# Performance work log

Hardware: AMD Instinct MI355X
Metric: run time of the kernel (lower is better)

The kernel has to match this reference:

```python
import jax, jax.numpy as jnp
import numpy as np

B, S, HID = 2, 2048, 2048
H, KV, D = 16, 4, 128          # query heads, kv heads, head_dim
G = H // KV                     # q heads per kv head
RD = 32                         # rotary_dim = int(0.25 * 128), even
THETA = 5000000.0
EPS = 1e-6


def _rms_norm(x, w):
    # out = x * rsqrt(mean(x^2)) * (1 + w)   (weight is zero-init)
    out = x * jax.lax.rsqrt(jnp.mean(x * x, axis=-1, keepdims=True) + EPS)
    return out * (1.0 + w.astype(x.dtype))


def _apply_rope(x, positions):
    # x: [B,S,h,RD]; standard HF rope with rotate_half on the rotary slice
    half = RD // 2
    inv_freq = 1.0 / (THETA ** (jnp.arange(0, half, dtype=jnp.float32) * 2.0 / RD))
    freqs = positions.astype(jnp.float32)[..., None] * inv_freq  # [B,S,half]
    emb = jnp.concatenate([freqs, freqs], axis=-1)               # [B,S,RD]
    cos = jnp.cos(emb)[:, :, None, :].astype(x.dtype)
    sin = jnp.sin(emb)[:, :, None, :].astype(x.dtype)
    x1, x2 = x[..., :half], x[..., half:]
    rot = jnp.concatenate([-x2, x1], axis=-1)
    return x * cos + rot * sin


def _partial_rope(q, k, positions):
    q_rot, q_pass = q[..., :RD], q[..., RD:]
    k_rot, k_pass = k[..., :RD], k[..., RD:]
    q_rot = _apply_rope(q_rot, positions)
    k_rot = _apply_rope(k_rot, positions)
    return (jnp.concatenate([q_rot, q_pass], axis=-1),
            jnp.concatenate([k_rot, k_pass], axis=-1))


def setup_inputs() -> dict:
    k0, k1, k2 = jax.random.split(jax.random.key(0), 3)
    x = jax.random.normal(k0, (B, S, HID), dtype=jnp.float32)
    positions = jnp.broadcast_to(jnp.arange(S, dtype=jnp.int32), (B, S))
    attention_mask = jnp.ones((B, S), dtype=bool)
    wqkv = jax.random.normal(k1, (HID, (H * 2 + 2 * KV) * D), dtype=jnp.float32) * 0.02
    wo = jax.random.normal(k2, (H * D, HID), dtype=jnp.float32) * 0.02
    q_norm_w = jnp.zeros((D,), dtype=jnp.float32)
    k_norm_w = jnp.zeros((D,), dtype=jnp.float32)
    return {"x": x, "positions": positions, "attention_mask": attention_mask,
            "wqkv": wqkv, "wo": wo, "q_norm_w": q_norm_w, "k_norm_w": k_norm_w}


def reference(x, positions, attention_mask, wqkv, wo, q_norm_w, k_norm_w):
    bsz, seq, _ = x.shape
    qkv = jnp.einsum('bsh,hf->bsf', x, wqkv)  # [B,S,5120]
    q_sz, kv_sz = H * 2 * D, KV * D
    q_raw = qkv[..., :q_sz]
    k_raw = qkv[..., q_sz:q_sz + kv_sz]
    v_raw = qkv[..., q_sz + kv_sz:]

    q_all = q_raw.reshape(bsz, seq, H, 2 * D)
    q, gate = jnp.split(q_all, 2, axis=-1)          # each [B,S,H,D]
    gate = gate.reshape(bsz, seq, H * D)

    q = _rms_norm(q, q_norm_w)
    k = _rms_norm(k_raw.reshape(bsz, seq, KV, D), k_norm_w)
    v = v_raw.reshape(bsz, seq, KV, D)
    q, k = _partial_rope(q, k, positions)

    # GQA causal attention, scale = 1/sqrt(head_dim)
    qg = q.reshape(bsz, seq, KV, G, D)
    scores = jnp.einsum('bqkgd,bskd->bkgqs', qg, k) * (1.0 / np.sqrt(D))
    causal = jnp.tril(jnp.ones((seq, seq), dtype=bool))
    mask = causal[None, None, None] & attention_mask[:, None, None, None, :]
    scores = jnp.where(mask, scores, jnp.finfo(scores.dtype).min)
    probs = jax.nn.softmax(scores, axis=-1)
    attn = jnp.einsum('bkgqs,bskd->bqkgd', probs, v)
    attn = attn.reshape(bsz, seq, H * D)

    attn = attn * jax.nn.sigmoid(gate)
    return jnp.einsum('bsf,fh->bsh', attn, wo)
```

## Files before the change

### kernel.cpp

```cpp
#include <hip/hip_runtime.h>

typedef unsigned short u16;
typedef unsigned int u32;
typedef __attribute__((ext_vector_type(8))) short short8;
typedef __attribute__((ext_vector_type(4))) float floatx4;

#define SEQ   2048
#define HIDD  2048
#define NQH   16
#define NKV   4
#define HDIM  128
#define QKV_N 5120
#define K_OFF 4096
#define V_OFF 4608
#define NTOK  4096
#define PSTR  40

__device__ __forceinline__ float b2f(u16 u) {
  u32 x = ((u32)u) << 16;
  return __builtin_bit_cast(float, x);
}
__device__ __forceinline__ u16 f2b(float f) {
  u32 x = __builtin_bit_cast(u32, f);
  u32 r = x + 0x7fffu + ((x >> 16) & 1u);
  return (u16)(r >> 16);
}
__device__ __forceinline__ short8 pack8(floatx4 a, floatx4 b) {
  short8 s;
#pragma unroll
  for (int j = 0; j < 4; j++) { s[j] = (short)f2b(a[j]); s[4 + j] = (short)f2b(b[j]); }
  return s;
}
__device__ __forceinline__ void async_copy16(const u16* g, u16* lds) {
  __builtin_amdgcn_global_load_lds((const __attribute__((address_space(1))) u32*)g,
                                   (__attribute__((address_space(3))) u32*)lds, 16, 0, 0);
}

__global__ __launch_bounds__(256) void cast_bf16(const float* __restrict__ in,
                                                 u16* __restrict__ out, int n8) {
  const int i = blockIdx.x * 256 + threadIdx.x;
  if (i < n8) {
    const floatx4 f0 = *(const floatx4*)(in + (size_t)i * 8);
    const floatx4 f1 = *(const floatx4*)(in + (size_t)i * 8 + 4);
    *(short8*)(out + (size_t)i * 8) = pack8(f0, f1);
  }
}

__global__ __launch_bounds__(256) void transpose_f32_bf16(const float* __restrict__ in,
                                                          u16* __restrict__ out,
                                                          int R, int C) {
  __shared__ float tile[32][33];
  const int bx = blockIdx.x * 32;
  const int by = blockIdx.y * 32;
  const int tx = threadIdx.x & 31;
  const int ty = threadIdx.x >> 5;
#pragma unroll
  for (int i = ty; i < 32; i += 8)
    tile[i][tx] = in[(size_t)(by + i) * C + bx + tx];
  __syncthreads();
#pragma unroll
  for (int i = ty; i < 32; i += 8)
    out[(size_t)(bx + i) * R + by + tx] = f2b(tile[tx][i]);
}

__global__ __launch_bounds__(256) void pack_kv(const u16* __restrict__ qkv,
                                               u16* __restrict__ Kc,
                                               u16* __restrict__ Vp) {
  __shared__ u16 tile[32][136];
  const int t0 = blockIdx.x * 32;
  const int kv = blockIdx.y;
  const int tid = threadIdx.x;
  const int b  = t0 / SEQ;
  const int tl = t0 - b * SEQ;
  const int jt = tl >> 5;
  const size_t kvbase = (size_t)(b * NKV + kv) * SEQ * HDIM;

  const int row  = tid >> 3;
  const int part = tid & 7;
  const size_t qbase = (size_t)(t0 + row) * QKV_N;
  const short8 kv0 = *(const short8*)(qkv + qbase + K_OFF + kv * HDIM + part * 16);
  const short8 kv1 = *(const short8*)(qkv + qbase + K_OFF + kv * HDIM + part * 16 + 8);
  *(short8*)(Kc + kvbase + (size_t)(tl + row) * HDIM + part * 16)     = kv0;
  *(short8*)(Kc + kvbase + (size_t)(tl + row) * HDIM + part * 16 + 8) = kv1;
  const short8 vv0 = *(const short8*)(qkv + qbase + V_OFF + kv * HDIM + part * 16);
  const short8 vv1 = *(const short8*)(qkv + qbase + V_OFF + kv * HDIM + part * 16 + 8);
  *(short8*)&tile[row][part * 16]     = vv0;
  *(short8*)&tile[row][part * 16 + 8] = vv1;
  __syncthreads();
  const int d = tid >> 1;
  const int half = tid & 1;
  u16* vout = Vp + kvbase + (size_t)jt * HDIM * 32 + d * 32 + half * 16;
  short8 o0;
#pragma unroll
  for (int i = 0; i < 8; i++) o0[i] = (short)tile[half * 16 + i][d];
  short8 o1;
#pragma unroll
  for (int i = 0; i < 8; i++) o1[i] = (short)tile[half * 16 + 8 + i][d];
  *(short8*)(vout) = o0;
  *(short8*)(vout + 8) = o1;
}

template <bool C32>
__global__ __launch_bounds__(512, 2) void gemm_bt8(const u16* __restrict__ A,
                                                   const u16* __restrict__ Bt,
                                                   void* __restrict__ Cp,
                                                   int M, int N, int K) {
  __shared__ __align__(16) u16 As[2][256 * 64];
  __shared__ __align__(16) u16 Bs[2][256 * 64];
  const int tid  = threadIdx.x;
  const int wave = tid >> 6;
  const int lane = tid & 63;
  const int lm   = lane & 15;
  const int lq   = lane >> 4;
  const int nwg = gridDim.x * gridDim.y;
  const int bid = blockIdx.y * gridDim.x + blockIdx.x;
  const int sbid = (bid & 7) * (nwg >> 3) + (bid >> 3);
  const int m0   = (sbid / gridDim.x) * 256;
  const int n0   = (sbid % gridDim.x) * 256;
  const int wr   = wave >> 2;
  const int wc   = wave & 3;
  const int NK   = K >> 6;

  const int r0 = wave * 16 + (lane >> 3);
  const int c0 = (((lane & 7) ^ (r0 & 7)) << 3);
  const int dls = wave * 1024;

  auto stageA = [&](int buf, int kt, int h) {
    const u16* g = A + (size_t)(m0 + h * 128 + r0) * K + kt * 64 + c0;
    async_copy16(g,                &As[buf][h * 8192 + dls]);
    async_copy16(g + (size_t)8 * K, &As[buf][h * 8192 + dls + 512]);
  };
  auto stageB = [&](int buf, int kt, int h) {
    const u16* g = Bt + (size_t)(n0 + h * 128 + r0) * K + kt * 64 + c0;
    async_copy16(g,                &Bs[buf][h * 8192 + dls]);
    async_copy16(g + (size_t)8 * K, &Bs[buf][h * 8192 + dls + 512]);
  };
  auto rdA = [&](int buf, int row, int ch) {
    return *(const short8*)&As[buf][row * 64 + ((ch ^ (row & 7)) << 3)];
  };
  auto rdB = [&](int buf, int row, int ch) {
    return *(const short8*)&Bs[buf][row * 64 + ((ch ^ (row & 7)) << 3)];
  };

  floatx4 acc[8][4] = {};
  short8 aF[4][2], bF[4][2];

  stageA(0, 0, 0); stageA(0, 0, 1);
  stageB(0, 0, 0); stageB(0, 0, 1);
  stageB(1, 1, 0); stageB(1, 1, 1);
  asm volatile("s_waitcnt vmcnt(4)" ::: "memory");
  __builtin_amdgcn_sched_barrier(0);
  __builtin_amdgcn_s_barrier();

  for (int j = 0; j < NK; ++j) {
    const int cur = j & 1;
#pragma unroll
    for (int m = 0; m < 4; ++m)
#pragma unroll
      for (int kk = 0; kk < 2; ++kk)
        aF[m][kk] = rdA(cur, wr * 128 + m * 16 + lm, kk * 4 + lq);
#pragma unroll
    for (int n = 0; n < 2; ++n)
#pragma unroll
      for (int kk = 0; kk < 2; ++kk)
        bF[n][kk] = rdB(cur, wc * 64 + n * 16 + lm, kk * 4 + lq);
    if (j + 1 < NK) stageA(cur ^ 1, j + 1, 0);
    __builtin_amdgcn_s_barrier();
    asm volatile("s_waitcnt lgkmcnt(0)" ::: "memory");
    __builtin_amdgcn_sched_barrier(0);
    __builtin_amdgcn_s_setprio(1);
#pragma unroll
    for (int m = 0; m < 4; ++m)
#pragma unroll
      for (int n = 0; n < 2; ++n)
#pragma unroll
        for (int kk = 0; kk < 2; ++kk)
          acc[m][n] = __builtin_amdgcn_mfma_f32_16x16x32_bf16(aF[m][kk], bF[n][kk], acc[m][n], 0, 0, 0);
    __builtin_amdgcn_s_setprio(0);
    __builtin_amdgcn_s_barrier();
#pragma unroll
    for (int n = 0; n < 2; ++n)
#pragma unroll
      for (int kk = 0; kk < 2; ++kk)
        bF[2 + n][kk] = rdB(cur, wc * 64 + (2 + n) * 16 + lm, kk * 4 + lq);
    if (j + 1 < NK) stageA(cur ^ 1, j + 1, 1);
    __builtin_amdgcn_s_barrier();
    asm volatile("s_waitcnt lgkmcnt(0)" ::: "memory");
    __builtin_amdgcn_sched_barrier(0);
    __builtin_amdgcn_s_setprio(1);
#pragma unroll
    for (int m = 0; m < 4; ++m)
#pragma unroll
      for (int n = 0; n < 2; ++n)
#pragma unroll
        for (int kk = 0; kk < 2; ++kk)
          acc[m][2 + n] = __builtin_amdgcn_mfma_f32_16x16x32_bf16(aF[m][kk], bF[2 + n][kk], acc[m][2 + n], 0, 0, 0);
    __builtin_amdgcn_s_setprio(0);
    __builtin_amdgcn_s_barrier();
#pragma unroll
    for (int m = 0; m < 4; ++m)
#pragma unroll
      for (int kk = 0; kk < 2; ++kk)
        aF[m][kk] = rdA(cur, wr * 128 + 64 + m * 16 + lm, kk * 4 + lq);
    if (j + 2 < NK) stageB(cur, j + 2, 0);
    __builtin_amdgcn_s_barrier();
    asm volatile("s_waitcnt lgkmcnt(0)" ::: "memory");
    __builtin_amdgcn_sched_barrier(0);
    __builtin_amdgcn_s_setprio(1);
#pragma unroll
    for (int m = 0; m < 4; ++m)
#pragma unroll
      for (int n = 0; n < 2; ++n)
#pragma unroll
        for (int kk = 0; kk < 2; ++kk)
          acc[4 + m][n] = __builtin_amdgcn_mfma_f32_16x16x32_bf16(aF[m][kk], bF[n][kk], acc[4 + m][n], 0, 0, 0);
    __builtin_amdgcn_s_setprio(0);
    __builtin_amdgcn_s_barrier();
    if (j + 2 < NK) stageB(cur, j + 2, 1);
    __builtin_amdgcn_s_barrier();
    __builtin_amdgcn_s_setprio(1);
#pragma unroll
    for (int m = 0; m < 4; ++m)
#pragma unroll
      for (int n = 0; n < 2; ++n)
#pragma unroll
        for (int kk = 0; kk < 2; ++kk)
          acc[4 + m][2 + n] = __builtin_amdgcn_mfma_f32_16x16x32_bf16(aF[m][kk], bF[2 + n][kk], acc[4 + m][2 + n], 0, 0, 0);
    __builtin_amdgcn_s_setprio(0);
    if (j + 2 < NK) asm volatile("s_waitcnt vmcnt(4)" ::: "memory");
    else            asm volatile("s_waitcnt vmcnt(0)" ::: "memory");
    __builtin_amdgcn_sched_barrier(0);
    __builtin_amdgcn_s_barrier();
  }

#pragma unroll
  for (int mi = 0; mi < 8; ++mi)
#pragma unroll
    for (int ni = 0; ni < 4; ++ni)
#pragma unroll
      for (int r = 0; r < 4; ++r) {
        const int row = m0 + wr * 128 + mi * 16 + lq * 4 + r;
        const int col = n0 + wc * 64 + ni * 16 + lm;
        if (C32) ((float*)Cp)[(size_t)row * N + col] = acc[mi][ni][r];
        else     ((u16*)Cp)[(size_t)row * N + col] = f2b(acc[mi][ni][r]);
      }
}

template <bool C32>
__global__ __launch_bounds__(512, 2) void gemm_n128(const u16* __restrict__ A,
                                                    const u16* __restrict__ Bt,
                                                    void* __restrict__ Cp,
                                                    int M, int N, int K) {
  __shared__ __align__(16) u16 As[2][256 * 64];
  __shared__ __align__(16) u16 Bs[2][128 * 64];
  const int tid  = threadIdx.x;
  const int wave = tid >> 6;
  const int lane = tid & 63;
  const int lm   = lane & 15;
  const int lq   = lane >> 4;
  const int nwg = gridDim.x * gridDim.y;
  const int bid = blockIdx.y * gridDim.x + blockIdx.x;
  const int sbid = (bid & 7) * (nwg >> 3) + (bid >> 3);
  const int m0   = (sbid / gridDim.x) * 256;
  const int n0   = (sbid % gridDim.x) * 128;
  const int wr   = wave >> 1;
  const int wc   = wave & 1;
  const int NK   = K >> 6;

  auto stA = [&](int buf, int kt, int L) {
    const int cd  = L * 512 + wave * 64 + lane;
    const int row = cd >> 3;
    const int ch  = cd & 7;
    async_copy16(A + (size_t)(m0 + row) * K + kt * 64 + ((ch ^ (row & 7)) << 3),
                 &As[buf][(L * 512 + wave * 64) * 8]);
  };
  auto stB = [&](int buf, int kt, int L) {
    const int cd  = L * 512 + wave * 64 + lane;
    const int row = cd >> 3;
    const int ch  = cd & 7;
    async_copy16(Bt + (size_t)(n0 + row) * K + kt * 64 + ((ch ^ (row & 7)) << 3),
                 &Bs[buf][(L * 512 + wave * 64) * 8]);
  };
  auto rdA = [&](int buf, int row, int ch) {
    return *(const short8*)&As[buf][row * 64 + ((ch ^ (row & 7)) << 3)];
  };
  auto rdB = [&](int buf, int row, int ch) {
    return *(const short8*)&Bs[buf][row * 64 + ((ch ^ (row & 7)) << 3)];
  };

  floatx4 acc[4][4] = {};
  short8 aF[4][2], bF[4][2];

  stA(0, 0, 0); stA(0, 0, 1); stA(0, 0, 2); stA(0, 0, 3);
  stB(0, 0, 0); stB(0, 0, 1);
  stB(1, 1, 0); stB(1, 1, 1);
  asm volatile("s_waitcnt vmcnt(2)" ::: "memory");
  __builtin_amdgcn_sched_barrier(0);
  __builtin_amdgcn_s_barrier();

  for (int j = 0; j < NK; ++j) {
    const int cur = j & 1;
#pragma unroll
    for (int m = 0; m < 4; ++m)
#pragma unroll
      for (int kk = 0; kk < 2; ++kk)
        aF[m][kk] = rdA(cur, wr * 64 + m * 16 + lm, kk * 4 + lq);
#pragma unroll
    for (int n = 0; n < 4; ++n)
#pragma unroll
      for (int kk = 0; kk < 2; ++kk)
        bF[n][kk] = rdB(cur, wc * 64 + n * 16 + lm, kk * 4 + lq);
    if (j + 1 < NK) { stA(cur ^ 1, j + 1, 0); stA(cur ^ 1, j + 1, 1); }
    asm volatile("s_waitcnt lgkmcnt(8)" ::: "memory");
    __builtin_amdgcn_s_barrier();
    asm volatile("s_waitcnt lgkmcnt(0)" ::: "memory");
    __builtin_amdgcn_sched_barrier(0);
    __builtin_amdgcn_s_setprio(1);
#pragma unroll
    for (int m = 0; m < 4; ++m)
#pragma unroll
      for (int n = 0; n < 2; ++n)
#pragma unroll
        for (int kk = 0; kk < 2; ++kk)
          acc[m][n] = __builtin_amdgcn_mfma_f32_16x16x32_bf16(aF[m][kk], bF[n][kk], acc[m][n], 0, 0, 0);
    __builtin_amdgcn_s_setprio(0);
    __builtin_amdgcn_s_barrier();
    if (j + 1 < NK) { stA(cur ^ 1, j + 1, 2); stA(cur ^ 1, j + 1, 3); }
    if (j + 2 < NK) { stB(cur, j + 2, 0); stB(cur, j + 2, 1); }
    __builtin_amdgcn_s_barrier();
    __builtin_amdgcn_sched_barrier(0);
    __builtin_amdgcn_s_setprio(1);
#pragma unroll
    for (int m = 0; m < 4; ++m)
#pragma unroll
      for (int n = 0; n < 2; ++n)
#pragma unroll
        for (int kk = 0; kk < 2; ++kk)
          acc[m][2 + n] = __builtin_amdgcn_mfma_f32_16x16x32_bf16(aF[m][kk], bF[2 + n][kk], acc[m][2 + n], 0, 0, 0);
    __builtin_amdgcn_s_setprio(0);
    if (j + 2 < NK) asm volatile("s_waitcnt vmcnt(2)" ::: "memory");
    else            asm volatile("s_waitcnt vmcnt(0)" ::: "memory");
    __builtin_amdgcn_sched_barrier(0);
    __builtin_amdgcn_s_barrier();
  }

#pragma unroll
  for (int mi = 0; mi < 4; ++mi)
#pragma unroll
    for (int ni = 0; ni < 4; ++ni)
#pragma unroll
      for (int r = 0; r < 4; ++r) {
        const int row = m0 + wr * 64 + mi * 16 + lq * 4 + r;
        const int col = n0 + wc * 64 + ni * 16 + lm;
        if (C32) ((float*)Cp)[(size_t)row * N + col] = acc[mi][ni][r];
        else     ((u16*)Cp)[(size_t)row * N + col] = f2b(acc[mi][ni][r]);
      }
}

__global__ __launch_bounds__(64) void postproc(u16* __restrict__ qkv,
                                               const int* __restrict__ positions,
                                               const float* __restrict__ qw,
                                               const float* __restrict__ kw) {
  const int tok  = blockIdx.x;
  const int u    = blockIdx.y;
  const int lane = threadIdx.x;
  const float* w;
  int base;
  if (u < NQH) { base = u * 256; w = qw; }
  else         { base = K_OFF + (u - NQH) * HDIM; w = kw; }
  u16* p = qkv + (size_t)tok * QKV_N + base;
  const int d0 = lane * 2;
  float v0 = b2f(p[d0]);
  float v1 = b2f(p[d0 + 1]);
  float ss = v0 * v0 + v1 * v1;
#pragma unroll
  for (int off = 32; off >= 1; off >>= 1) ss += __shfl_xor(ss, off, 64);
  const float rs = rsqrtf(ss * (1.0f / 128.0f) + 1e-6f);
  v0 = v0 * rs * (1.0f + w[d0]);
  v1 = v1 * rs * (1.0f + w[d0 + 1]);
  const float pv0 = __shfl_xor(v0, 8, 64);
  const float pv1 = __shfl_xor(v1, 8, 64);
  if (d0 < 32) {
    const float fpos = (float)positions[tok];
    const int i = d0 & 15;
    const float inv0 = __powf(5.0e6f, -((float)i) / 16.0f);
    const float inv1 = __powf(5.0e6f, -((float)(i + 1)) / 16.0f);
    float s0, c0, s1, c1;
    sincosf(fpos * inv0, &s0, &c0);
    sincosf(fpos * inv1, &s1, &c1);
    if (d0 < 16) { v0 = v0 * c0 - pv0 * s0; v1 = v1 * c1 - pv1 * s1; }
    else         { v0 = v0 * c0 + pv0 * s0; v1 = v1 * c1 + pv1 * s1; }
  }
  if (u < NQH) {
    v0 *= 0.08838834764831845f;
    v1 *= 0.08838834764831845f;
  }
  p[d0]     = f2b(v0);
  p[d0 + 1] = f2b(v1);
}

__global__ __launch_bounds__(256) void attn_kernel(const u16* __restrict__ qkv,
                                                   const u16* __restrict__ Kc,
                                                   const u16* __restrict__ Vp,
                                                   u16* __restrict__ attn_g) {
  __shared__ __align__(16) u16 Ks[2][4][32][32];
  __shared__ __align__(16) u16 Vs[2][128][32];
  __shared__ __align__(16) u16 P_lds[4][16 * PSTR];
  const int tid  = threadIdx.x;
  const int wave = tid >> 6;
  const int lane = tid & 63;
  const int lm = lane & 15;
  const int lq = lane >> 4;
  const int kvi = blockIdx.y;
  const int b   = blockIdx.z;
  const int h   = kvi * 4 + wave;
  const size_t tokbase = (size_t)b * SEQ;
  const size_t kvbase  = (size_t)(b * NKV + kvi) * SEQ * HDIM;
  const int klocal = lane >> 2;
  const int ssw = ((lane & 3) ^ ((lane >> 3) & 3)) * 8;
  const int rsw = (lq ^ ((lm >> 1) & 3)) * 8;

  short8 onesF;
#pragma unroll
  for (int j = 0; j < 8; j++) onesF[j] = (short)0x3F80;

  auto stage = [&](int buf, int j) {
    const u16* ksrc = Kc + kvbase + (size_t)j * 32 * HDIM;
#pragma unroll
    for (int half = 0; half < 2; half++)
      async_copy16(ksrc + (size_t)(half * 16 + klocal) * HDIM + wave * 32 + ssw,
                   &Ks[buf][wave][half * 16][0]);
    const u16* vsrc = Vp + kvbase + (size_t)j * (HDIM * 32);
#pragma unroll
    for (int i = 0; i < 2; i++)
      async_copy16(vsrc + wave * 1024 + i * 512 + (lane >> 2) * 32 + ssw,
                   &Vs[buf][wave * 32 + i * 16][0]);
  };

  auto run_tile = [&](int t) {
    short8 qF[4];
    const u16* qp = qkv + (tokbase + 16 * t + lm) * QKV_N + h * 256;
#pragma unroll
    for (int kc = 0; kc < 4; kc++)
      qF[kc] = *(const short8*)(qp + kc * 32 + lq * 8);

    floatx4 O[8] = {};
    floatx4 lacc = {};
    const int jmax = t >> 1;
    const int moff = (t & 1) * 16;

    __syncthreads();
    stage(0, 0);
    for (int j = 0; j <= jmax; j++) {
      const int cur = j & 1;
      __syncthreads();
      if (j < jmax) stage(cur ^ 1, j + 1);
      short8 kF[2][4], vF[8];
#pragma unroll
      for (int n0 = 0; n0 < 2; n0++)
#pragma unroll
        for (int kc = 0; kc < 4; kc++)
          kF[n0][kc] = *(const short8*)&Ks[cur][kc][n0 * 16 + lm][rsw];
#pragma unroll
      for (int dc = 0; dc < 8; dc++)
        vF[dc] = *(const short8*)&Vs[cur][dc * 16 + lm][rsw];

      floatx4 Sc[2] = {};
#pragma unroll
      for (int n0 = 0; n0 < 2; n0++)
#pragma unroll
        for (int kc = 0; kc < 4; kc++)
          Sc[n0] = __builtin_amdgcn_mfma_f32_16x16x32_bf16(qF[kc], kF[n0][kc], Sc[n0], 0, 0, 0);

      const bool masked = (j == jmax);
#pragma unroll
      for (int n0 = 0; n0 < 2; n0++)
#pragma unroll
        for (int r = 0; r < 4; r++) {
          float pe = __expf(Sc[n0][r]);
          if (masked) {
            const int rowloc = lq * 4 + r;
            const int keyloc = n0 * 16 + lm;
            pe = (keyloc <= rowloc + moff) ? pe : 0.0f;
          }
          P_lds[wave][(lq * 4 + r) * PSTR + n0 * 16 + lm] = f2b(pe);
        }
      const short8 pF = *(const short8*)&P_lds[wave][lm * PSTR + lq * 8];
      lacc = __builtin_amdgcn_mfma_f32_16x16x32_bf16(pF, onesF, lacc, 0, 0, 0);
#pragma unroll
      for (int dc = 0; dc < 8; dc++)
        O[dc] = __builtin_amdgcn_mfma_f32_16x16x32_bf16(pF, vF[dc], O[dc], 0, 0, 0);
    }

#pragma unroll
    for (int r = 0; r < 4; r++) {
      const int row = 16 * t + lq * 4 + r;
      const size_t tok = tokbase + row;
      const float inv_l = 1.0f / lacc[r];
#pragma unroll
      for (int dc = 0; dc < 8; dc++) {
        const int d = dc * 16 + lm;
        const float g = b2f(qkv[tok * QKV_N + h * 256 + 128 + d]);
        const float sg = 1.0f / (1.0f + __expf(-g));
        attn_g[tok * HIDD + h * HDIM + d] = f2b(O[dc][r] * inv_l * sg);
      }
    }
  };

  const int p = blockIdx.x;
  run_tile(p);
  run_tile(127 - p);
}

extern "C" void kernel_launch(void* const* d_in, const int* in_sizes, int n_in,
                              void* d_out, int out_size, void* d_ws, size_t ws_size,
                              hipStream_t stream) {
  const float* x        = (const float*)d_in[0];
  const int* positions  = (const int*)d_in[1];
  const float* wqkv     = (const float*)d_in[3];
  const float* wo       = (const float*)d_in[4];
  const float* qnw      = (const float*)d_in[5];
  const float* knw      = (const float*)d_in[6];
  float* out = (float*)d_out;

  char* ws = (char*)d_ws;
  u16* qkv    = (u16*)(ws);
  u16* wqkv_t = (u16*)(ws + 41943040);
  u16* attn_g = (u16*)(ws + 41943040);
  u16* Kc     = (u16*)(ws + 58720256);
  u16* wo_t   = (u16*)(ws);
  u16* xb     = (u16*)d_out;
  u16* Vp     = (u16*)d_out;

  cast_bf16<<<dim3(NTOK * HIDD / 8 / 256), 256, 0, stream>>>(x, xb, NTOK * HIDD / 8);
  transpose_f32_bf16<<<dim3(QKV_N / 32, HIDD / 32), 256, 0, stream>>>(wqkv, wqkv_t, HIDD, QKV_N);
  gemm_bt8<false><<<dim3(QKV_N / 256, NTOK / 256), 512, 0, stream>>>(xb, wqkv_t, qkv, NTOK, QKV_N, HIDD);
  postproc<<<dim3(NTOK, NQH + NKV), 64, 0, stream>>>(qkv, positions, qnw, knw);
  pack_kv<<<dim3(NTOK / 32, NKV), 256, 0, stream>>>(qkv, Kc, Vp);
  attn_kernel<<<dim3(64, NKV, 2), 256, 0, stream>>>(qkv, Kc, Vp, attn_g);
  transpose_f32_bf16<<<dim3(HIDD / 32, HIDD / 32), 256, 0, stream>>>(wo, wo_t, HIDD, HIDD);
  gemm_n128<true><<<dim3(HIDD / 128, NTOK / 256), 512, 0, stream>>>(attn_g, wo_t, out, NTOK, HIDD, HIDD);
}
```

Measured before the change: 432.7 us.

## Split QKV GEMM into big-tile Q part and small-tile KV part; batch postproc tokens

The QKV projection GEMM is split in two. The first 4096 output columns use the 256x256 tiled kernel, and the remaining 1024 K/V columns use a new simple 128x128 kernel writing with a leading dimension. This is meant to fix the tile quantization at N=5120, which is not a multiple of 256 (5120/256=20 works, but the grid is 20x16=320 blocks, which is uneven against the CU count). The postproc kernel now handles 16 tokens per 256-thread block, with weights and inverse frequencies hoisted out of the token loop, which cuts launch and block overhead. A partial lgkmcnt wait is added before the barrier in the big GEMM. The new 128 kernel is unpipelined, so it may run slowly on its own.

```diff
diff --git a/kernel.cpp b/kernel.cpp
--- a/kernel.cpp
+++ b/kernel.cpp
@@ -104,7 +104,7 @@
 __global__ __launch_bounds__(512, 2) void gemm_bt8(const u16* __restrict__ A,
                                                    const u16* __restrict__ Bt,
                                                    void* __restrict__ Cp,
-                                                   int M, int N, int K) {
+                                                   int M, int N, int K, int ldc) {
   __shared__ __align__(16) u16 As[2][256 * 64];
   __shared__ __align__(16) u16 Bs[2][256 * 64];
   const int tid  = threadIdx.x;
@@ -165,6 +165,7 @@
       for (int kk = 0; kk < 2; ++kk)
         bF[n][kk] = rdB(cur, wc * 64 + n * 16 + lm, kk * 4 + lq);
     if (j + 1 < NK) stageA(cur ^ 1, j + 1, 0);
+    asm volatile("s_waitcnt lgkmcnt(8)" ::: "memory");
     __builtin_amdgcn_s_barrier();
     asm volatile("s_waitcnt lgkmcnt(0)" ::: "memory");
     __builtin_amdgcn_sched_barrier(0);
@@ -241,8 +242,64 @@
       for (int r = 0; r < 4; ++r) {
         const int row = m0 + wr * 128 + mi * 16 + lq * 4 + r;
         const int col = n0 + wc * 64 + ni * 16 + lm;
-        if (C32) ((float*)Cp)[(size_t)row * N + col] = acc[mi][ni][r];
-        else     ((u16*)Cp)[(size_t)row * N + col] = f2b(acc[mi][ni][r]);
+        if (C32) ((float*)Cp)[(size_t)row * ldc + col] = acc[mi][ni][r];
+        else     ((u16*)Cp)[(size_t)row * ldc + col] = f2b(acc[mi][ni][r]);
+      }
+}
+
+template <bool C32>
+__global__ __launch_bounds__(256) void gemm_bt128(const u16* __restrict__ A,
+                                                  const u16* __restrict__ Bt,
+                                                  void* __restrict__ Cp,
+                                                  int M, int N, int K, int ldc) {
+  __shared__ __align__(16) u16 As[128 * 32];
+  __shared__ __align__(16) u16 Bs[128 * 32];
+  const int tid  = threadIdx.x;
+  const int wave = tid >> 6;
+  const int lane = tid & 63;
+  const int m0 = blockIdx.y * 128;
+  const int n0 = blockIdx.x * 128;
+  const int wr = wave >> 1, wc = wave & 1;
+  const int lrow = lane >> 2;
+  const int lcol = (lane & 3) * 8;
+  const int lm = lane & 15;
+  const int lq = lane >> 4;
+
+  floatx4 acc[4][4] = {};
+
+  for (int k0 = 0; k0 < K; k0 += 32) {
+#pragma unroll
+    for (int i = 0; i < 2; i++) {
+      const int r = wave * 32 + i * 16;
+      async_copy16(A  + (size_t)(m0 + r + lrow) * K + k0 + lcol, &As[r * 32]);
+      async_copy16(Bt + (size_t)(n0 + r + lrow) * K + k0 + lcol, &Bs[r * 32]);
+    }
+    __syncthreads();
+    short8 aF[4], bF[4];
+#pragma unroll
+    for (int mi = 0; mi < 4; mi++)
+      aF[mi] = *(const short8*)&As[(wr * 64 + mi * 16 + lm) * 32 + lq * 8];
+#pragma unroll
+    for (int ni = 0; ni < 4; ni++)
+      bF[ni] = *(const short8*)&Bs[(wc * 64 + ni * 16 + lm) * 32 + lq * 8];
+#pragma unroll
+    for (int mi = 0; mi < 4; mi++)
+#pragma unroll
+      for (int ni = 0; ni < 4; ni++)
+        acc[mi][ni] = __builtin_amdgcn_mfma_f32_16x16x32_bf16(aF[mi], bF[ni], acc[mi][ni], 0, 0, 0);
+    __syncthreads();
+  }
+
+#pragma unroll
+  for (int mi = 0; mi < 4; mi++)
+#pragma unroll
+    for (int ni = 0; ni < 4; ni++)
+#pragma unroll
+      for (int r = 0; r < 4; r++) {
+        const int row = m0 + wr * 64 + mi * 16 + lq * 4 + r;
+        const int col = n0 + wc * 64 + ni * 16 + lm;
+        if (C32) ((float*)Cp)[(size_t)row * ldc + col] = acc[mi][ni][r];
+        else     ((u16*)Cp)[(size_t)row * ldc + col] = f2b(acc[mi][ni][r]);
       }
 }
 
@@ -250,7 +307,7 @@
 __global__ __launch_bounds__(512, 2) void gemm_n128(const u16* __restrict__ A,
                                                     const u16* __restrict__ Bt,
                                                     void* __restrict__ Cp,
-                                                    int M, int N, int K) {
+                                                    int M, int N, int K, int ldc) {
   __shared__ __align__(16) u16 As[2][256 * 64];
   __shared__ __align__(16) u16 Bs[2][128 * 64];
   const int tid  = threadIdx.x;
@@ -352,51 +409,57 @@
       for (int r = 0; r < 4; ++r) {
         const int row = m0 + wr * 64 + mi * 16 + lq * 4 + r;
         const int col = n0 + wc * 64 + ni * 16 + lm;
-        if (C32) ((float*)Cp)[(size_t)row * N + col] = acc[mi][ni][r];
-        else     ((u16*)Cp)[(size_t)row * N + col] = f2b(acc[mi][ni][r]);
+        if (C32) ((float*)Cp)[(size_t)row * ldc + col] = acc[mi][ni][r];
+        else     ((u16*)Cp)[(size_t)row * ldc + col] = f2b(acc[mi][ni][r]);
       }
 }
 
-__global__ __launch_bounds__(64) void postproc(u16* __restrict__ qkv,
-                                               const int* __restrict__ positions,
-                                               const float* __restrict__ qw,
-                                               const float* __restrict__ kw) {
-  const int tok  = blockIdx.x;
+__global__ __launch_bounds__(256) void postproc(u16* __restrict__ qkv,
+                                                const int* __restrict__ positions,
+                                                const float* __restrict__ qw,
+                                                const float* __restrict__ kw) {
   const int u    = blockIdx.y;
-  const int lane = threadIdx.x;
+  const int wv   = threadIdx.x >> 6;
+  const int lane = threadIdx.x & 63;
   const float* w;
   int base;
   if (u < NQH) { base = u * 256; w = qw; }
   else         { base = K_OFF + (u - NQH) * HDIM; w = kw; }
-  u16* p = qkv + (size_t)tok * QKV_N + base;
   const int d0 = lane * 2;
-  float v0 = b2f(p[d0]);
-  float v1 = b2f(p[d0 + 1]);
-  float ss = v0 * v0 + v1 * v1;
-#pragma unroll
-  for (int off = 32; off >= 1; off >>= 1) ss += __shfl_xor(ss, off, 64);
-  const float rs = rsqrtf(ss * (1.0f / 128.0f) + 1e-6f);
-  v0 = v0 * rs * (1.0f + w[d0]);
-  v1 = v1 * rs * (1.0f + w[d0 + 1]);
-  const float pv0 = __shfl_xor(v0, 8, 64);
-  const float pv1 = __shfl_xor(v1, 8, 64);
+  const float w0 = 1.0f + w[d0];
+  const float w1 = 1.0f + w[d0 + 1];
+  float inv0 = 0.0f, inv1 = 0.0f;
   if (d0 < 32) {
-    const float fpos = (float)positions[tok];
     const int i = d0 & 15;
-    const float inv0 = __powf(5.0e6f, -((float)i) / 16.0f);
-    const float inv1 = __powf(5.0e6f, -((float)(i + 1)) / 16.0f);
-    float s0, c0, s1, c1;
-    sincosf(fpos * inv0, &s0, &c0);
-    sincosf(fpos * inv1, &s1, &c1);
-    if (d0 < 16) { v0 = v0 * c0 - pv0 * s0; v1 = v1 * c1 - pv1 * s1; }
-    else         { v0 = v0 * c0 + pv0 * s0; v1 = v1 * c1 + pv1 * s1; }
+    inv0 = __powf(5.0e6f, -((float)i) / 16.0f);
+    inv1 = __powf(5.0e6f, -((float)(i + 1)) / 16.0f);
   }
-  if (u < NQH) {
-    v0 *= 0.08838834764831845f;
-    v1 *= 0.08838834764831845f;
+  const float qsc = (u < NQH) ? 0.08838834764831845f : 1.0f;
+#pragma unroll
+  for (int it = 0; it < 4; ++it) {
+    const int tok = blockIdx.x * 16 + wv * 4 + it;
+    u16* p = qkv + (size_t)tok * QKV_N + base;
+    float v0 = b2f(p[d0]);
+    float v1 = b2f(p[d0 + 1]);
+    float ss = v0 * v0 + v1 * v1;
+#pragma unroll
+    for (int off = 32; off >= 1; off >>= 1) ss += __shfl_xor(ss, off, 64);
+    const float rs = rsqrtf(ss * (1.0f / 128.0f) + 1e-6f);
+    v0 = v0 * rs * w0;
+    v1 = v1 * rs * w1;
+    const float pv0 = __shfl_xor(v0, 8, 64);
+    const float pv1 = __shfl_xor(v1, 8, 64);
+    if (d0 < 32) {
+      const float fpos = (float)positions[tok];
+      float s0, c0, s1, c1;
+      sincosf(fpos * inv0, &s0, &c0);
+      sincosf(fpos * inv1, &s1, &c1);
+      if (d0 < 16) { v0 = v0 * c0 - pv0 * s0; v1 = v1 * c1 - pv1 * s1; }
+      else         { v0 = v0 * c0 + pv0 * s0; v1 = v1 * c1 + pv1 * s1; }
+    }
+    p[d0]     = f2b(v0 * qsc);
+    p[d0 + 1] = f2b(v1 * qsc);
   }
-  p[d0]     = f2b(v0);
-  p[d0 + 1] = f2b(v1);
 }
 
 __global__ __launch_bounds__(256) void attn_kernel(const u16* __restrict__ qkv,
@@ -534,10 +597,14 @@
 
   cast_bf16<<<dim3(NTOK * HIDD / 8 / 256), 256, 0, stream>>>(x, xb, NTOK * HIDD / 8);
   transpose_f32_bf16<<<dim3(QKV_N / 32, HIDD / 32), 256, 0, stream>>>(wqkv, wqkv_t, HIDD, QKV_N);
-  gemm_bt8<false><<<dim3(QKV_N / 256, NTOK / 256), 512, 0, stream>>>(xb, wqkv_t, qkv, NTOK, QKV_N, HIDD);
-  postproc<<<dim3(NTOK, NQH + NKV), 64, 0, stream>>>(qkv, positions, qnw, knw);
+  gemm_bt8<false><<<dim3(4096 / 256, NTOK / 256), 512, 0, stream>>>(
+      xb, wqkv_t, qkv, NTOK, 4096, HIDD, QKV_N);
+  gemm_bt128<false><<<dim3(1024 / 128, NTOK / 128), 256, 0, stream>>>(
+      xb, wqkv_t + (size_t)4096 * HIDD, qkv + 4096, NTOK, 1024, HIDD, QKV_N);
+  postproc<<<dim3(NTOK / 16, NQH + NKV), 256, 0, stream>>>(qkv, positions, qnw, knw);
   pack_kv<<<dim3(NTOK / 32, NKV), 256, 0, stream>>>(qkv, Kc, Vp);
   attn_kernel<<<dim3(64, NKV, 2), 256, 0, stream>>>(qkv, Kc, Vp, attn_g);
   transpose_f32_bf16<<<dim3(HIDD / 32, HIDD / 32), 256, 0, stream>>>(wo, wo_t, HIDD, HIDD);
-  gemm_n128<true><<<dim3(HIDD / 128, NTOK / 256), 512, 0, stream>>>(attn_g, wo_t, out, NTOK, HIDD, HIDD);
-}
+  gemm_n128<true><<<dim3(HIDD / 128, NTOK / 256), 512, 0, stream>>>(
+      attn_g, wo_t, out, NTOK, HIDD, HIDD, HIDD);
+}
```

Result: faster. 397.6 us (-8.1%).
